# Performance work log

Measured on AMD Instinct MI355X. Metric: run time of the kernel, lower is better.

## Reference

```python
import jax, jax.numpy as jnp
import numpy as np

B, N, C = 256, 25, 256          # batch, joints, in_features
H = 256                          # hidden_features (MLP hidden = H // 2 = 128)


def _build_chain_paths(n):
    """Flatten shortest paths of a chain skeleton (parent[i]=i-1) into
    (heads, ends, pair_ids): edge k of path i->j contributes
    src[:, ends[e]] - src[:, heads[e]] accumulated into pair i*n+j."""
    heads, ends, pair = [], [], []
    for i in range(n):
        for j in range(n):
            step = 1 if j >= i else -1
            cur = i
            while cur != j:
                heads.append(cur)
                ends.append(cur + step)
                pair.append(i * n + j)
                cur += step
    return (np.asarray(heads, np.int32), np.asarray(ends, np.int32),
            np.asarray(pair, np.int32))


def setup_inputs() -> dict:
    key = jax.random.key(0)
    k_src, k_w1, k_w2 = jax.random.split(key, 3)
    heads, ends, pair_ids = _build_chain_paths(N)  # E = 5200 for N=25
    src = jax.random.normal(k_src, (B, N, C), dtype=jnp.float32)
    # torch Linear weights: [out, in], no bias for both edgefeat linears
    W1 = jax.random.normal(k_w1, (H // 2, C), dtype=jnp.float32) / np.sqrt(C)
    W2 = jax.random.normal(k_w2, (1, H // 2), dtype=jnp.float32) / np.sqrt(H // 2)
    alpha = jnp.full((1,), 0.25, dtype=jnp.float32)  # PReLU init
    return {"src": src, "heads": jnp.asarray(heads), "ends": jnp.asarray(ends),
            "pair_ids": jnp.asarray(pair_ids), "W1": W1, "alpha": alpha, "W2": W2}


def reference(src, heads, ends, pair_ids, W1, alpha, W2):
    b, n, c = src.shape
    # gather-subtract along every path edge: [B, E, C]
    diff = src[:, ends, :] - src[:, heads, :]
    # accumulate per (i, j) pair: segment_sum over leading axis -> [N*N, B, C]
    acc = jax.ops.segment_sum(jnp.transpose(diff, (1, 0, 2)), pair_ids,
                              num_segments=n * n)
    edge_feat = jnp.transpose(acc.reshape(n, n, b, c), (2, 0, 1, 3))  # [B,N,N,C]
    h = jnp.einsum('bijc,hc->bijh', edge_feat, W1)   # [B,N,N,H//2]
    h = jnp.where(h >= 0, h, alpha * h)              # PReLU (single shared alpha)
    return jnp.einsum('bijh,oh->bijo', h, W2)        # [B,N,N,1]
```

## Files before the change

### kernel.cpp

```cpp
#include <hip/hip_runtime.h>

#define NJ   25
#define CIN  256
#define HH   128
#define SS   264
#define US   136

typedef _Float16 h2  __attribute__((ext_vector_type(2)));
typedef _Float16 h8f __attribute__((ext_vector_type(8)));
typedef __attribute__((ext_vector_type(4))) float f32x4;

__device__ __forceinline__ unsigned short f2h_bits(float f) {
    union { _Float16 h; unsigned short u; } v; v.h = (_Float16)f; return v.u;
}
__device__ __forceinline__ unsigned pack2h(float a, float b) {
    return (unsigned)f2h_bits(a) | ((unsigned)f2h_bits(b) << 16);
}
__device__ __forceinline__ h2 as_h2(unsigned u) {
    union { unsigned u; h2 h; } v; v.u = u; return v.h;
}

__global__ __launch_bounds__(512) void fused_edge_mlp_v9(
    const float* __restrict__ src,
    const float* __restrict__ W1,
    const float* __restrict__ Aarr,
    const float* __restrict__ W2,
    float* __restrict__ out)
{
    __shared__ unsigned short w1_lds[HH * SS];
    __shared__ unsigned short s_lds[NJ * SS];
    __shared__ unsigned short u16[NJ * US];
    __shared__ unsigned w2s[HH / 2];
    __shared__ float s_s[NJ];

    const int b    = blockIdx.x;
    const int t    = threadIdx.x;
    const int w    = t >> 6;
    const int lane = t & 63;
    const int ln15 = lane & 15;
    const int quad = lane >> 4;
    const int hcol = w * 16 + ln15;

    {
        const float4* w4 = (const float4*)W1;
        #pragma unroll 4
        for (int idx = t; idx < HH * CIN / 4; idx += 512) {
            const int r = idx >> 6, k4 = idx & 63;
            float4 v = w4[idx];
            *(uint2*)&w1_lds[r * SS + k4 * 4] =
                make_uint2(pack2h(v.x, v.y), pack2h(v.z, v.w));
        }
        const float4* s4 = (const float4*)(src + (size_t)b * NJ * CIN);
        for (int idx = t; idx < NJ * CIN / 4; idx += 512) {
            const int n = idx >> 6, k4 = idx & 63;
            float4 v = s4[idx];
            *(uint2*)&s_lds[n * SS + k4 * 4] =
                make_uint2(pack2h(v.x, v.y), pack2h(v.z, v.w));
        }
        if (t < HH / 2) w2s[t] = pack2h(W2[2 * t], W2[2 * t + 1]);
    }
    __syncthreads();

    {
        const int r1    = 16 + ln15;
        const bool r1ok = (r1 < NJ);
        const int cbase = quad * 8;

        f32x4 acc0 = {0.f, 0.f, 0.f, 0.f};
        f32x4 acc1 = {0.f, 0.f, 0.f, 0.f};
        #pragma unroll
        for (int kt = 0; kt < 8; ++kt) {
            const int co = kt * 32 + cbase;
            h8f bf = *(const h8f*)&w1_lds[hcol * SS + co];
            h8f a0 = *(const h8f*)&s_lds[ln15 * SS + co];
            h8f a1 = {};
            if (r1ok) a1 = *(const h8f*)&s_lds[r1 * SS + co];
            acc0 = __builtin_amdgcn_mfma_f32_16x16x32_f16(a0, bf, acc0, 0, 0, 0);
            acc1 = __builtin_amdgcn_mfma_f32_16x16x32_f16(a1, bf, acc1, 0, 0, 0);
        }

        #pragma unroll
        for (int r = 0; r < 4; ++r) {
            int m0 = quad * 4 + r;
            if (m0 < NJ) u16[m0 * US + hcol] = f2h_bits(acc0[r]);
            int m1 = 16 + quad * 4 + r;
            if (m1 < NJ) u16[m1 * US + hcol] = f2h_bits(acc1[r]);
        }
    }
    __syncthreads();

    const float alpha = Aarr[0];
    float* outb = out + (size_t)b * (NJ * NJ);
    const uint4* w2v = (const uint4*)w2s;

    float M = 0.f;
    int i = 0, j = 0;
    if (t < 300) {
        i = (int)((49.0f - sqrtf(2401.0f - 8.0f * (float)t)) * 0.5f);
        {
            int Si = (49 * i - i * i) >> 1;
            if (t < Si) { --i; }
            else { int Sn = (49 * (i + 1) - (i + 1) * (i + 1)) >> 1; if (t >= Sn) ++i; }
        }
        const int S = (49 * i - i * i) >> 1;
        j = t - S + i + 1;

        const uint4* ujp = (const uint4*)(u16 + j * US);
        const uint4* uip = (const uint4*)(u16 + i * US);
        #pragma unroll
        for (int h8 = 0; h8 < 16; ++h8) {
            uint4 a = ujp[h8], c = uip[h8], ww = w2v[h8];
            h2 mx;
            mx = __builtin_elementwise_max(as_h2(a.x), as_h2(c.x));
            M  = __builtin_amdgcn_fdot2(mx, as_h2(ww.x), M, false);
            mx = __builtin_elementwise_max(as_h2(a.y), as_h2(c.y));
            M  = __builtin_amdgcn_fdot2(mx, as_h2(ww.y), M, false);
            mx = __builtin_elementwise_max(as_h2(a.z), as_h2(c.z));
            M  = __builtin_amdgcn_fdot2(mx, as_h2(ww.z), M, false);
            mx = __builtin_elementwise_max(as_h2(a.w), as_h2(c.w));
            M  = __builtin_amdgcn_fdot2(mx, as_h2(ww.w), M, false);
        }
    } else if (t < 300 + NJ) {
        const int r = t - 300;
        const uint4* up = (const uint4*)(u16 + r * US);
        float s = 0.f;
        #pragma unroll
        for (int h8 = 0; h8 < 16; ++h8) {
            uint4 a = up[h8], ww = w2v[h8];
            s = __builtin_amdgcn_fdot2(as_h2(a.x), as_h2(ww.x), s, false);
            s = __builtin_amdgcn_fdot2(as_h2(a.y), as_h2(ww.y), s, false);
            s = __builtin_amdgcn_fdot2(as_h2(a.z), as_h2(ww.z), s, false);
            s = __builtin_amdgcn_fdot2(as_h2(a.w), as_h2(ww.w), s, false);
        }
        s_s[r] = s;
    }
    __syncthreads();

    if (t < 300) {
        const float sj = s_s[j], si = s_s[i];
        const float Mw = (1.f - alpha) * M;
        outb[i * NJ + j] = Mw + alpha * sj - si;
        outb[j * NJ + i] = Mw + alpha * si - sj;
    } else if (t >= 325 && t < 350) {
        const int r = t - 325;
        outb[r * (NJ + 1)] = 0.f;
    }
}

extern "C" void kernel_launch(void* const* d_in, const int* in_sizes, int n_in,
                              void* d_out, int out_size, void* d_ws, size_t ws_size,
                              hipStream_t stream) {
    const float* src   = (const float*)d_in[0];
    const float* W1    = (const float*)d_in[4];
    const float* alpha = (const float*)d_in[5];
    const float* W2    = (const float*)d_in[6];
    float* out = (float*)d_out;

    const int B = in_sizes[0] / (NJ * CIN);
    fused_edge_mlp_v9<<<B, 512, 0, stream>>>(src, W1, alpha, W2, out);
}
```

Before: 71.92 us.

## Load W1 fragments straight into registers instead of staging through LDS

Each thread now loads its own W1 MFMA B-operand fragment directly from global memory into registers and converts it to fp16 there, which removes the 64KB shared-memory W1 staging buffer and its LDS reads and writes. The src loads are also issued all at once before the LDS stores so more memory requests are in flight together. The smaller LDS footprint could let more blocks fit per CU. The cost is higher register use (64 floats for W1 plus the src prefetch) and less coalesced, 32-byte strided global reads of W1.

```diff
diff --git a/kernel.cpp b/kernel.cpp
--- a/kernel.cpp
+++ b/kernel.cpp
@@ -20,14 +20,13 @@
     union { unsigned u; h2 h; } v; v.u = u; return v.h;
 }
 
-__global__ __launch_bounds__(512) void fused_edge_mlp_v9(
+__global__ __launch_bounds__(512) void fused_edge_mlp_v10(
     const float* __restrict__ src,
     const float* __restrict__ W1,
     const float* __restrict__ Aarr,
     const float* __restrict__ W2,
     float* __restrict__ out)
 {
-    __shared__ unsigned short w1_lds[HH * SS];
     __shared__ unsigned short s_lds[NJ * SS];
     __shared__ unsigned short u16[NJ * US];
     __shared__ unsigned w2s[HH / 2];
@@ -41,23 +40,43 @@
     const int quad = lane >> 4;
     const int hcol = w * 16 + ln15;
 
-    {
-        const float4* w4 = (const float4*)W1;
-        #pragma unroll 4
-        for (int idx = t; idx < HH * CIN / 4; idx += 512) {
-            const int r = idx >> 6, k4 = idx & 63;
-            float4 v = w4[idx];
-            *(uint2*)&w1_lds[r * SS + k4 * 4] =
-                make_uint2(pack2h(v.x, v.y), pack2h(v.z, v.w));
+    const float* w1row = W1 + (size_t)hcol * CIN + quad * 8;
+    float4 w1r[16];
+    #pragma unroll
+    for (int kt = 0; kt < 8; ++kt) {
+        w1r[2 * kt]     = *(const float4*)(w1row + kt * 32);
+        w1r[2 * kt + 1] = *(const float4*)(w1row + kt * 32 + 4);
+    }
+
+    const float4* s4 = (const float4*)(src + (size_t)b * NJ * CIN);
+    float4 sv[4];
+    #pragma unroll
+    for (int it = 0; it < 4; ++it) {
+        const int idx = t + it * 512;
+        if (idx < NJ * CIN / 4) sv[it] = s4[idx];
+    }
+    if (t < HH / 2) w2s[t] = pack2h(W2[2 * t], W2[2 * t + 1]);
+
+    #pragma unroll
+    for (int it = 0; it < 4; ++it) {
+        const int idx = t + it * 512;
+        if (idx < NJ * CIN / 4) {
+            const int n = idx >> 6, k4 = idx & 63;
+            *(uint2*)&s_lds[n * SS + k4 * 4] =
+                make_uint2(pack2h(sv[it].x, sv[it].y), pack2h(sv[it].z, sv[it].w));
         }
-        const float4* s4 = (const float4*)(src + (size_t)b * NJ * CIN);
-        for (int idx = t; idx < NJ * CIN / 4; idx += 512) {
-            const int n = idx >> 6, k4 = idx & 63;
-            float4 v = s4[idx];
-            *(uint2*)&s_lds[n * SS + k4 * 4] =
-                make_uint2(pack2h(v.x, v.y), pack2h(v.z, v.w));
-        }
-        if (t < HH / 2) w2s[t] = pack2h(W2[2 * t], W2[2 * t + 1]);
+    }
+
+    h8f bfr[8];
+    #pragma unroll
+    for (int kt = 0; kt < 8; ++kt) {
+        const float4 lo = w1r[2 * kt], hi = w1r[2 * kt + 1];
+        h8f f;
+        f[0] = (_Float16)lo.x; f[1] = (_Float16)lo.y;
+        f[2] = (_Float16)lo.z; f[3] = (_Float16)lo.w;
+        f[4] = (_Float16)hi.x; f[5] = (_Float16)hi.y;
+        f[6] = (_Float16)hi.z; f[7] = (_Float16)hi.w;
+        bfr[kt] = f;
     }
     __syncthreads();
 
@@ -71,12 +90,11 @@
         #pragma unroll
         for (int kt = 0; kt < 8; ++kt) {
             const int co = kt * 32 + cbase;
-            h8f bf = *(const h8f*)&w1_lds[hcol * SS + co];
             h8f a0 = *(const h8f*)&s_lds[ln15 * SS + co];
             h8f a1 = {};
             if (r1ok) a1 = *(const h8f*)&s_lds[r1 * SS + co];
-            acc0 = __builtin_amdgcn_mfma_f32_16x16x32_f16(a0, bf, acc0, 0, 0, 0);
-            acc1 = __builtin_amdgcn_mfma_f32_16x16x32_f16(a1, bf, acc1, 0, 0, 0);
+            acc0 = __builtin_amdgcn_mfma_f32_16x16x32_f16(a0, bfr[kt], acc0, 0, 0, 0);
+            acc1 = __builtin_amdgcn_mfma_f32_16x16x32_f16(a1, bfr[kt], acc1, 0, 0, 0);
         }
 
         #pragma unroll
@@ -157,5 +175,5 @@
     float* out = (float*)d_out;
 
     const int B = in_sizes[0] / (NJ * CIN);
-    fused_edge_mlp_v9<<<B, 512, 0, stream>>>(src, W1, alpha, W2, out);
+    fused_edge_mlp_v10<<<B, 512, 0, stream>>>(src, W1, alpha, W2, out);
 }
```

New measurement: 72.14 us. Within noise of the previous version (+0.3%).
